# Kernel tuning notes

Hardware: AMD Instinct MI355X
Metric: run time of the kernel (lower is better)

Reference implementation:

```python
import jax, jax.numpy as jnp
import numpy as np

N, IN_DIM, INTER, HID, OUT, G = 8192, 512, 512, 1024, 512, 16
EPS = 1e-5


def setup_inputs() -> dict:
    key = jax.random.key(0)
    ks = jax.random.split(key, 16)
    s = 0.02
    return {
        "h": jax.random.normal(ks[0], (N, IN_DIM), jnp.float32),
        "D": jax.random.uniform(ks[1], (N, N), jnp.float32),
        "h_prime": jax.random.normal(ks[2], (N, OUT), jnp.float32),
        "Qw": jax.random.normal(ks[3], (IN_DIM, INTER), jnp.float32) * s,
        "Qb": jnp.zeros((INTER,), jnp.float32),
        "Kw": jax.random.normal(ks[4], (IN_DIM, INTER), jnp.float32) * s,
        "Kb": jnp.zeros((INTER,), jnp.float32),
        "Vw": jax.random.normal(ks[5], (IN_DIM, INTER), jnp.float32) * s,
        "Vb": jnp.zeros((INTER,), jnp.float32),
        "Rw": jax.random.normal(ks[6], (INTER, HID), jnp.float32) * s,
        "Rb": jnp.zeros((HID,), jnp.float32),
        "Cw": jax.random.normal(ks[7], (OUT, HID), jnp.float32) * s,
        "Cb": jnp.zeros((HID,), jnp.float32),
        "Pw": jax.random.normal(ks[8], (2 * HID, OUT), jnp.float32) * s,
        "Pb": jnp.zeros((OUT,), jnp.float32),
        "prelu_a": jnp.full((OUT,), 0.25, jnp.float32),  # PReLU default init
        "gn_w": jnp.ones((OUT,), jnp.float32),
        "gn_b": jnp.zeros((OUT,), jnp.float32),
    }


def reference(h, D, h_prime, Qw, Qb, Kw, Kb, Vw, Vb, Rw, Rb, Cw, Cb, Pw, Pb, prelu_a, gn_w, gn_b):
    Q = h @ Qw + Qb                      # (N, inter)
    K = h @ Kw + Kb
    V = h @ Vw + Vb
    scores = D * (Q @ K.T)               # (N, N), decayed retention scores
    h_ret = scores @ V                   # (N, inter)
    h_ret = jax.nn.gelu(h_ret @ Rw + Rb, approximate=False)   # (N, hid)
    h_cat = h_prime @ Cw + Cb            # (N, hid)
    combined = jnp.concatenate([h_ret, h_cat], axis=-1)       # (N, 2*hid)
    x = combined @ Pw + Pb               # (N, out)
    x = jnp.where(x >= 0, x, prelu_a * x)                      # PReLU per-channel
    # GroupNorm over channel groups per row: (N, G, out/G)
    xg = x.reshape(N, G, OUT // G)
    mu = xg.mean(axis=-1, keepdims=True)
    var = xg.var(axis=-1, keepdims=True)
    xn = ((xg - mu) * jax.lax.rsqrt(var + EPS)).reshape(N, OUT)
    return xn * gn_w + gn_b
```

## Files before the change

### kernel.cpp

```cpp
#include <hip/hip_runtime.h>
#include <math.h>

typedef __attribute__((ext_vector_type(8))) short bf16x8;
typedef __attribute__((ext_vector_type(4))) float f32x4;
typedef __attribute__((ext_vector_type(8))) unsigned short u16x8;

#define DEVFN __device__ __forceinline__

DEVFN unsigned short f2bf(float f) {
    unsigned int u = __float_as_uint(f);
    u += 0x7fffu + ((u >> 16) & 1u);
    return (unsigned short)(u >> 16);
}

__global__ void cast_f32_bf16_kernel(const float* __restrict__ in,
                                     unsigned short* __restrict__ out, int n8) {
    int i = blockIdx.x * blockDim.x + threadIdx.x;
    if (i >= n8) return;
    const float4* p = reinterpret_cast<const float4*>(in) + (size_t)i * 2;
    float4 a = p[0], b = p[1];
    u16x8 o;
    o[0] = f2bf(a.x); o[1] = f2bf(a.y); o[2] = f2bf(a.z); o[3] = f2bf(a.w);
    o[4] = f2bf(b.x); o[5] = f2bf(b.y); o[6] = f2bf(b.z); o[7] = f2bf(b.w);
    reinterpret_cast<u16x8*>(out)[i] = o;
}

__global__ void sum4_cast_kernel(const float* __restrict__ p, size_t stride,
                                 unsigned short* __restrict__ out, int n8) {
    int i = blockIdx.x * blockDim.x + threadIdx.x;
    if (i >= n8) return;
    const float4* a = reinterpret_cast<const float4*>(p) + (size_t)i * 2;
    const float4* b = reinterpret_cast<const float4*>(p + stride) + (size_t)i * 2;
    const float4* c = reinterpret_cast<const float4*>(p + 2 * stride) + (size_t)i * 2;
    const float4* d = reinterpret_cast<const float4*>(p + 3 * stride) + (size_t)i * 2;
    u16x8 o;
#pragma unroll
    for (int j = 0; j < 2; ++j) {
        float4 va = a[j], vb = b[j], vc = c[j], vd = d[j];
        o[4 * j + 0] = f2bf(va.x + vb.x + vc.x + vd.x);
        o[4 * j + 1] = f2bf(va.y + vb.y + vc.y + vd.y);
        o[4 * j + 2] = f2bf(va.z + vb.z + vc.z + vd.z);
        o[4 * j + 3] = f2bf(va.w + vb.w + vc.w + vd.w);
    }
    reinterpret_cast<u16x8*>(out)[i] = o;
}

__global__ void concat_bias_kernel(const float* __restrict__ a,
                                   const float* __restrict__ b,
                                   const float* __restrict__ c,
                                   float* __restrict__ o) {
    int i = blockIdx.x * blockDim.x + threadIdx.x;
    if (i >= 1536) return;
    o[i] = i < 512 ? a[i] : (i < 1024 ? b[i - 512] : c[i - 1024]);
}

DEVFN unsigned short to_bf16_bits(float f) { return f2bf(f); }
DEVFN unsigned short to_bf16_bits(unsigned short u) { return u; }

template <typename T>
__global__ void transpose_to_bf16_kernel(const T* __restrict__ in, int ldin,
                                         unsigned short* __restrict__ out, int ldout) {
    __shared__ unsigned short tile[32][34];
    int c0 = blockIdx.x * 32, r0 = blockIdx.y * 32;
    int tx = threadIdx.x, ty = threadIdx.y;
#pragma unroll
    for (int i = 0; i < 32; i += 8)
        tile[ty + i][tx] = to_bf16_bits(in[(size_t)(r0 + ty + i) * ldin + c0 + tx]);
    __syncthreads();
#pragma unroll
    for (int i = 0; i < 32; i += 8)
        out[(size_t)(c0 + ty + i) * ldout + r0 + tx] = tile[tx][ty + i];
}

enum { EP_BF16_BIAS = 0, EP_BF16_DMUL = 1, EP_BF16_GELU = 2, EP_F32 = 3, EP_PRELU_GN = 4 };

template <int MODE>
__global__ __launch_bounds__(256) void gemm_bt_kernel(
    const unsigned short* __restrict__ A, int lda,
    const unsigned short* __restrict__ B, int ldb,
    void* __restrict__ Cv, int ldc, int K,
    const float* __restrict__ bias,
    const float* __restrict__ Dmul, int ldd,
    const float* __restrict__ PA, const float* __restrict__ GW,
    const float* __restrict__ GB, size_t zstride) {
    __shared__ alignas(16) unsigned short As[128 * 64];
    __shared__ alignas(16) unsigned short Bs[128 * 64];

    unsigned nwg = gridDim.x * gridDim.y;
    unsigned bid = blockIdx.y * gridDim.x + blockIdx.x;
    unsigned cpx = nwg >> 3;
    bid = (bid & 7u) * cpx + (bid >> 3);
    unsigned bx = bid % gridDim.x, by = bid / gridDim.x;
    size_t m0 = (size_t)by * 128, n0 = (size_t)bx * 128;

    size_t koff = (size_t)blockIdx.z * K;
    A += koff;
    B += koff;

    int tid = threadIdx.x;
    int lane = tid & 63, w = tid >> 6;
    int wr = w >> 1, wc = w & 1;

    f32x4 acc[4][4];
#pragma unroll
    for (int i = 0; i < 4; ++i)
#pragma unroll
        for (int j = 0; j < 4; ++j)
#pragma unroll
            for (int r = 0; r < 4; ++r) acc[i][j][r] = 0.f;

    const unsigned short* Ablk = A + m0 * lda;
    const unsigned short* Bblk = B + n0 * ldb;
    int srccol = ((lane & 7) ^ (lane >> 3)) * 8;
    int srow = w * 32 + (lane >> 3);
    unsigned short* ldsA = As + w * 2048;
    unsigned short* ldsB = Bs + w * 2048;

    int nkt = K >> 6;
    for (int kt = 0; kt < nkt; ++kt) {
        int k0 = kt << 6;
#pragma unroll
        for (int i = 0; i < 4; ++i) {
            __builtin_amdgcn_global_load_lds(
                (const __attribute__((address_space(1))) void*)(Ablk + (size_t)(srow + i * 8) * lda + k0 + srccol),
                (__attribute__((address_space(3))) void*)(ldsA + i * 512), 16, 0, 0);
            __builtin_amdgcn_global_load_lds(
                (const __attribute__((address_space(1))) void*)(Bblk + (size_t)(srow + i * 8) * ldb + k0 + srccol),
                (__attribute__((address_space(3))) void*)(ldsB + i * 512), 16, 0, 0);
        }
        __syncthreads();

        const bf16x8* Ap = reinterpret_cast<const bf16x8*>(As);
        const bf16x8* Bp = reinterpret_cast<const bf16x8*>(Bs);
#pragma unroll
        for (int kk = 0; kk < 2; ++kk) {
            bf16x8 af[4], bfr[4];
#pragma unroll
            for (int mi = 0; mi < 4; ++mi) {
                int row = wr * 64 + mi * 16 + (lane & 15);
                int slot = ((kk << 2) + (lane >> 4)) ^ (row & 7);
                af[mi] = Ap[row * 8 + slot];
            }
#pragma unroll
            for (int ni = 0; ni < 4; ++ni) {
                int row = wc * 64 + ni * 16 + (lane & 15);
                int slot = ((kk << 2) + (lane >> 4)) ^ (row & 7);
                bfr[ni] = Bp[row * 8 + slot];
            }
#pragma unroll
            for (int mi = 0; mi < 4; ++mi)
#pragma unroll
                for (int ni = 0; ni < 4; ++ni)
                    acc[mi][ni] = __builtin_amdgcn_mfma_f32_16x16x32_bf16(
                        af[mi], bfr[ni], acc[mi][ni], 0, 0, 0);
        }
        __syncthreads();
    }

    int cif = lane & 15;
    int rif = (lane >> 4) << 2;

    if (MODE == EP_PRELU_GN) {
        float* Cf = (float*)Cv;
        float pbv[4], pav[4], gwv[4], gbv[4];
        size_t gcolv[4];
#pragma unroll
        for (int ni = 0; ni < 4; ++ni) {
            gcolv[ni] = n0 + wc * 64 + ni * 16 + cif;
            pbv[ni] = bias[gcolv[ni]];
            pav[ni] = PA[gcolv[ni]];
            gwv[ni] = GW[gcolv[ni]];
            gbv[ni] = GB[gcolv[ni]];
        }
#pragma unroll
        for (int mi = 0; mi < 4; ++mi) {
#pragma unroll
            for (int ni = 0; ni < 4; ++ni)
#pragma unroll
                for (int r = 0; r < 4; ++r) {
                    float v = acc[mi][ni][r] + pbv[ni];
                    acc[mi][ni][r] = v >= 0.f ? v : pav[ni] * v;
                }
#pragma unroll
            for (int p = 0; p < 2; ++p) {
                float s[4], ss[4];
#pragma unroll
                for (int r = 0; r < 4; ++r) {
                    float a0 = acc[mi][2 * p][r], a1 = acc[mi][2 * p + 1][r];
                    s[r] = a0 + a1;
                    ss[r] = a0 * a0 + a1 * a1;
                }
#pragma unroll
                for (int msk = 1; msk < 16; msk <<= 1)
#pragma unroll
                    for (int r = 0; r < 4; ++r) {
                        s[r] += __shfl_xor(s[r], msk);
                        ss[r] += __shfl_xor(ss[r], msk);
                    }
#pragma unroll
                for (int r = 0; r < 4; ++r) {
                    float mu = s[r] * (1.f / 32.f);
                    float inv = rsqrtf(ss[r] * (1.f / 32.f) - mu * mu + 1e-5f);
                    size_t grow = m0 + wr * 64 + mi * 16 + rif + r;
#pragma unroll
                    for (int q = 0; q < 2; ++q) {
                        int ni = 2 * p + q;
                        Cf[grow * (size_t)ldc + gcolv[ni]] =
                            (acc[mi][ni][r] - mu) * inv * gwv[ni] + gbv[ni];
                    }
                }
            }
        }
        return;
    }

#pragma unroll
    for (int mi = 0; mi < 4; ++mi) {
#pragma unroll
        for (int ni = 0; ni < 4; ++ni) {
            size_t gcol = n0 + wc * 64 + ni * 16 + cif;
            float bval = 0.f;
            if (MODE == EP_BF16_BIAS || MODE == EP_BF16_GELU || MODE == EP_F32)
                if (bias) bval = bias[gcol];
#pragma unroll
            for (int r = 0; r < 4; ++r) {
                size_t grow = m0 + wr * 64 + mi * 16 + rif + r;
                float val = acc[mi][ni][r] + bval;
                if (MODE == EP_BF16_DMUL)
                    val = acc[mi][ni][r] * Dmul[grow * (size_t)ldd + gcol];
                if (MODE == EP_BF16_GELU)
                    val = 0.5f * val * (1.f + erff(val * 0.70710678118654752f));
                if (MODE == EP_F32) {
                    float* Cf = (float*)Cv + blockIdx.z * zstride;
                    Cf[grow * (size_t)ldc + gcol] = val;
                } else {
                    ((unsigned short*)Cv)[grow * (size_t)ldc + gcol] = f2bf(val);
                }
            }
        }
    }
}

extern "C" void kernel_launch(void* const* d_in, const int* in_sizes, int n_in,
                              void* d_out, int out_size, void* d_ws, size_t ws_size,
                              hipStream_t stream) {
    constexpr int Nn = 8192, IND = 512, INTER = 512, HID = 1024, OUTD = 512;
    const float* h   = (const float*)d_in[0];
    const float* Dm  = (const float*)d_in[1];
    const float* hp  = (const float*)d_in[2];
    const float* Qw  = (const float*)d_in[3];
    const float* Qb  = (const float*)d_in[4];
    const float* Kw  = (const float*)d_in[5];
    const float* Kb  = (const float*)d_in[6];
    const float* Vw  = (const float*)d_in[7];
    const float* Vb  = (const float*)d_in[8];
    const float* Rw  = (const float*)d_in[9];
    const float* Rb  = (const float*)d_in[10];
    const float* Cw  = (const float*)d_in[11];
    const float* Cb  = (const float*)d_in[12];
    const float* Pw  = (const float*)d_in[13];
    const float* Pb  = (const float*)d_in[14];
    const float* pa  = (const float*)d_in[15];
    const float* gwt = (const float*)d_in[16];
    const float* gbt = (const float*)d_in[17];
    (void)in_sizes; (void)n_in; (void)out_size; (void)ws_size;

    char* ws = (char*)d_ws;
    size_t cur = 0;
    auto alloc = [&](size_t bytes) -> void* {
        void* p = ws + cur;
        cur += (bytes + 255) & ~(size_t)255;
        return p;
    };
    unsigned short* h_bf   = (unsigned short*)alloc((size_t)Nn * IND * 2);
    unsigned short* hp_bf  = (unsigned short*)alloc((size_t)Nn * OUTD * 2);
    unsigned short* QKVwT  = (unsigned short*)alloc((size_t)3 * INTER * IND * 2);
    float*          qkvb   = (float*)alloc((size_t)3 * INTER * 4);
    unsigned short* RwT    = (unsigned short*)alloc((size_t)INTER * HID * 2);
    unsigned short* CwT    = (unsigned short*)alloc((size_t)OUTD * HID * 2);
    unsigned short* PwT    = (unsigned short*)alloc((size_t)2 * HID * OUTD * 2);
    unsigned short* QKVm   = (unsigned short*)alloc((size_t)Nn * 3 * INTER * 2);
    unsigned short* VTm    = (unsigned short*)alloc((size_t)Nn * INTER * 2);
    unsigned short* Sm     = (unsigned short*)alloc((size_t)Nn * Nn * 2);
    float*          hret32 = (float*)alloc((size_t)4 * Nn * INTER * 4);
    unsigned short* hretbf = (unsigned short*)alloc((size_t)Nn * INTER * 2);
    unsigned short* comb   = Sm;

    unsigned short* Qm = QKVm;
    unsigned short* Km = QKVm + INTER;
    unsigned short* Vm = QKVm + 2 * INTER;
    const int ldqkv = 3 * INTER;

    dim3 tb(32, 8);
    int n8 = Nn * IND / 8;
    cast_f32_bf16_kernel<<<n8 / 256, 256, 0, stream>>>(h, h_bf, n8);
    cast_f32_bf16_kernel<<<n8 / 256, 256, 0, stream>>>(hp, hp_bf, n8);
    transpose_to_bf16_kernel<float><<<dim3(INTER / 32, IND / 32), tb, 0, stream>>>(Qw, INTER, QKVwT, IND);
    transpose_to_bf16_kernel<float><<<dim3(INTER / 32, IND / 32), tb, 0, stream>>>(Kw, INTER, QKVwT + (size_t)INTER * IND, IND);
    transpose_to_bf16_kernel<float><<<dim3(INTER / 32, IND / 32), tb, 0, stream>>>(Vw, INTER, QKVwT + (size_t)2 * INTER * IND, IND);
    concat_bias_kernel<<<6, 256, 0, stream>>>(Qb, Kb, Vb, qkvb);
    transpose_to_bf16_kernel<float><<<dim3(HID / 32, INTER / 32), tb, 0, stream>>>(Rw, HID, RwT, INTER);
    transpose_to_bf16_kernel<float><<<dim3(HID / 32, OUTD / 32), tb, 0, stream>>>(Cw, HID, CwT, OUTD);
    transpose_to_bf16_kernel<float><<<dim3(OUTD / 32, 2 * HID / 32), tb, 0, stream>>>(Pw, OUTD, PwT, 2 * HID);

    gemm_bt_kernel<EP_BF16_BIAS><<<dim3(3 * INTER / 128, Nn / 128), 256, 0, stream>>>(
        h_bf, IND, QKVwT, IND, QKVm, ldqkv, IND, qkvb, nullptr, 0, nullptr, nullptr, nullptr, 0);
    transpose_to_bf16_kernel<unsigned short><<<dim3(INTER / 32, Nn / 32), tb, 0, stream>>>(Vm, ldqkv, VTm, Nn);

    gemm_bt_kernel<EP_BF16_DMUL><<<dim3(Nn / 128, Nn / 128), 256, 0, stream>>>(
        Qm, ldqkv, Km, ldqkv, Sm, Nn, INTER, nullptr, Dm, Nn, nullptr, nullptr, nullptr, 0);

    gemm_bt_kernel<EP_F32><<<dim3(OUTD / 128, Nn / 128, 4), 256, 0, stream>>>(
        Sm, Nn, VTm, Nn, hret32, INTER, Nn / 4, nullptr, nullptr, 0,
        nullptr, nullptr, nullptr, (size_t)Nn * INTER);
    sum4_cast_kernel<<<(Nn * INTER / 8) / 256, 256, 0, stream>>>(
        hret32, (size_t)Nn * INTER, hretbf, Nn * INTER / 8);

    gemm_bt_kernel<EP_BF16_GELU><<<dim3(HID / 128, Nn / 128), 256, 0, stream>>>(
        hretbf, INTER, RwT, INTER, comb, 2 * HID, INTER, Rb, nullptr, 0, nullptr, nullptr, nullptr, 0);
    gemm_bt_kernel<EP_BF16_BIAS><<<dim3(HID / 128, Nn / 128), 256, 0, stream>>>(
        hp_bf, OUTD, CwT, OUTD, comb + HID, 2 * HID, OUTD, Cb, nullptr, 0, nullptr, nullptr, nullptr, 0);

    gemm_bt_kernel<EP_PRELU_GN><<<dim3(OUTD / 128, Nn / 128), 256, 0, stream>>>(
        comb, 2 * HID, PwT, 2 * HID, d_out, OUTD, 2 * HID, Pb, nullptr, 0, pa, gwt, gbt, 0);
}
```

Baseline: 450.7 us.

## Double-buffer GEMM LDS, prefetch D, merge launches, remap split-K blocks

The GEMM kernel now double-buffers its LDS tiles so the next K-tile's global-to-LDS loads overlap the MFMA work on the current tile. In the score GEMM, the D-matrix elements are prefetched into registers during the last K iteration instead of being loaded in the epilogue. Split-K blocks are remapped across XCDs, and launch_bounds now requests 2 blocks per CU. Several small launches are merged: two casts into one, six weight transposes into one, and the R and C GEMMs into a single dual-mode launch. This doubles LDS use to 64KB per block and adds 64 prefetch registers per thread, which may limit occupancy.

```diff
diff --git a/kernel.cpp b/kernel.cpp
--- a/kernel.cpp
+++ b/kernel.cpp
@@ -13,15 +13,18 @@
     return (unsigned short)(u >> 16);
 }
 
-__global__ void cast_f32_bf16_kernel(const float* __restrict__ in,
-                                     unsigned short* __restrict__ out, int n8) {
+__global__ void cast2_kernel(const float* __restrict__ a, const float* __restrict__ b,
+                             unsigned short* __restrict__ oa, unsigned short* __restrict__ ob,
+                             int n8) {
+    const float* in = blockIdx.y ? b : a;
+    unsigned short* out = blockIdx.y ? ob : oa;
     int i = blockIdx.x * blockDim.x + threadIdx.x;
     if (i >= n8) return;
     const float4* p = reinterpret_cast<const float4*>(in) + (size_t)i * 2;
-    float4 a = p[0], b = p[1];
+    float4 x = p[0], y = p[1];
     u16x8 o;
-    o[0] = f2bf(a.x); o[1] = f2bf(a.y); o[2] = f2bf(a.z); o[3] = f2bf(a.w);
-    o[4] = f2bf(b.x); o[5] = f2bf(b.y); o[6] = f2bf(b.z); o[7] = f2bf(b.w);
+    o[0] = f2bf(x.x); o[1] = f2bf(x.y); o[2] = f2bf(x.z); o[3] = f2bf(x.w);
+    o[4] = f2bf(y.x); o[5] = f2bf(y.y); o[6] = f2bf(y.z); o[7] = f2bf(y.w);
     reinterpret_cast<u16x8*>(out)[i] = o;
 }
 
@@ -54,52 +57,97 @@
     o[i] = i < 512 ? a[i] : (i < 1024 ? b[i - 512] : c[i - 1024]);
 }
 
-DEVFN unsigned short to_bf16_bits(float f) { return f2bf(f); }
-DEVFN unsigned short to_bf16_bits(unsigned short u) { return u; }
-
-template <typename T>
-__global__ void transpose_to_bf16_kernel(const T* __restrict__ in, int ldin,
-                                         unsigned short* __restrict__ out, int ldout) {
+struct TD { const float* in; unsigned short* out; int ldin, ldout, nbx, nby; };
+struct TD6 { TD d[6]; };
+
+__global__ void multi_transpose_kernel(TD6 t6) {
+    TD d = t6.d[blockIdx.z];
+    if ((int)blockIdx.x >= d.nbx || (int)blockIdx.y >= d.nby) return;
     __shared__ unsigned short tile[32][34];
     int c0 = blockIdx.x * 32, r0 = blockIdx.y * 32;
     int tx = threadIdx.x, ty = threadIdx.y;
 #pragma unroll
     for (int i = 0; i < 32; i += 8)
-        tile[ty + i][tx] = to_bf16_bits(in[(size_t)(r0 + ty + i) * ldin + c0 + tx]);
+        tile[ty + i][tx] = f2bf(d.in[(size_t)(r0 + ty + i) * d.ldin + c0 + tx]);
+    __syncthreads();
+#pragma unroll
+    for (int i = 0; i < 32; i += 8)
+        d.out[(size_t)(c0 + ty + i) * d.ldout + r0 + tx] = tile[tx][ty + i];
+}
+
+__global__ void transpose_bf16_kernel(const unsigned short* __restrict__ in, int ldin,
+                                      unsigned short* __restrict__ out, int ldout) {
+    __shared__ unsigned short tile[32][34];
+    int c0 = blockIdx.x * 32, r0 = blockIdx.y * 32;
+    int tx = threadIdx.x, ty = threadIdx.y;
+#pragma unroll
+    for (int i = 0; i < 32; i += 8)
+        tile[ty + i][tx] = in[(size_t)(r0 + ty + i) * ldin + c0 + tx];
     __syncthreads();
 #pragma unroll
     for (int i = 0; i < 32; i += 8)
         out[(size_t)(c0 + ty + i) * ldout + r0 + tx] = tile[tx][ty + i];
 }
 
-enum { EP_BF16_BIAS = 0, EP_BF16_DMUL = 1, EP_BF16_GELU = 2, EP_F32 = 3, EP_PRELU_GN = 4 };
+enum { EP_BF16_BIAS = 0, EP_BF16_DMUL = 1, EP_F32 = 3, EP_PRELU_GN = 4, EP_DUAL = 5 };
 
 template <int MODE>
-__global__ __launch_bounds__(256) void gemm_bt_kernel(
+__global__ __launch_bounds__(256, 2) void gemm_bt_kernel(
     const unsigned short* __restrict__ A, int lda,
     const unsigned short* __restrict__ B, int ldb,
     void* __restrict__ Cv, int ldc, int K,
     const float* __restrict__ bias,
     const float* __restrict__ Dmul, int ldd,
     const float* __restrict__ PA, const float* __restrict__ GW,
-    const float* __restrict__ GB, size_t zstride) {
-    __shared__ alignas(16) unsigned short As[128 * 64];
-    __shared__ alignas(16) unsigned short Bs[128 * 64];
-
-    unsigned nwg = gridDim.x * gridDim.y;
-    unsigned bid = blockIdx.y * gridDim.x + blockIdx.x;
-    unsigned cpx = nwg >> 3;
-    bid = (bid & 7u) * cpx + (bid >> 3);
-    unsigned bx = bid % gridDim.x, by = bid / gridDim.x;
-    size_t m0 = (size_t)by * 128, n0 = (size_t)bx * 128;
-
-    size_t koff = (size_t)blockIdx.z * K;
-    A += koff;
-    B += koff;
+    const float* __restrict__ GB, size_t zstride,
+    const unsigned short* __restrict__ A2,
+    const unsigned short* __restrict__ B2,
+    const float* __restrict__ bias2) {
+    __shared__ alignas(16) unsigned short As[2][128 * 64];
+    __shared__ alignas(16) unsigned short Bs[2][128 * 64];
+
+    unsigned bx, by, zi;
+    if (MODE == EP_F32) {
+        unsigned gx = gridDim.x;
+        unsigned L = (blockIdx.z * gridDim.y + blockIdx.y) * gx + blockIdx.x;
+        unsigned xcd = L & 7u, slot = L >> 3;
+        zi = xcd >> 1;
+        unsigned t = slot * 2 + (xcd & 1u);
+        bx = t & (gx - 1);
+        by = t / gx;
+    } else {
+        unsigned nwg = gridDim.x * gridDim.y;
+        unsigned bid = blockIdx.y * gridDim.x + blockIdx.x;
+        unsigned cpx = nwg >> 3;
+        bid = (bid & 7u) * cpx + (bid >> 3);
+        bx = bid % gridDim.x;
+        by = bid / gridDim.x;
+        zi = 0;
+    }
+    size_t m0 = (size_t)by * 128;
+    size_t nB = (size_t)bx * 128;
+    size_t ncol0 = nB;
+
+    const unsigned short* Ause = A;
+    const unsigned short* Buse = B;
+    const float* bias_use = bias;
+    bool apply_gelu = false;
+    if (MODE == EP_DUAL) {
+        unsigned half = gridDim.x >> 1;
+        if (bx >= half) {
+            nB = (size_t)(bx - half) * 128;
+            ncol0 = 1024 + nB;
+            Ause = A2; Buse = B2; bias_use = bias2;
+        } else {
+            apply_gelu = true;
+        }
+    }
 
     int tid = threadIdx.x;
     int lane = tid & 63, w = tid >> 6;
     int wr = w >> 1, wc = w & 1;
+    int cif = lane & 15;
+    int rif = (lane >> 4) << 2;
 
     f32x4 acc[4][4];
 #pragma unroll
@@ -109,29 +157,50 @@
 #pragma unroll
             for (int r = 0; r < 4; ++r) acc[i][j][r] = 0.f;
 
-    const unsigned short* Ablk = A + m0 * lda;
-    const unsigned short* Bblk = B + n0 * ldb;
+    const unsigned short* Ablk = Ause + m0 * lda + (size_t)zi * K;
+    const unsigned short* Bblk = Buse + nB * ldb + (size_t)zi * K;
     int srccol = ((lane & 7) ^ (lane >> 3)) * 8;
     int srow = w * 32 + (lane >> 3);
-    unsigned short* ldsA = As + w * 2048;
-    unsigned short* ldsB = Bs + w * 2048;
-
     int nkt = K >> 6;
-    for (int kt = 0; kt < nkt; ++kt) {
+
+    float dreg[4][4][4];
+
+    auto stage = [&](int buf, int kt) {
         int k0 = kt << 6;
+        unsigned short* la = &As[buf][w * 2048];
+        unsigned short* lb = &Bs[buf][w * 2048];
 #pragma unroll
         for (int i = 0; i < 4; ++i) {
             __builtin_amdgcn_global_load_lds(
                 (const __attribute__((address_space(1))) void*)(Ablk + (size_t)(srow + i * 8) * lda + k0 + srccol),
-                (__attribute__((address_space(3))) void*)(ldsA + i * 512), 16, 0, 0);
+                (__attribute__((address_space(3))) void*)(la + i * 512), 16, 0, 0);
             __builtin_amdgcn_global_load_lds(
                 (const __attribute__((address_space(1))) void*)(Bblk + (size_t)(srow + i * 8) * ldb + k0 + srccol),
-                (__attribute__((address_space(3))) void*)(ldsB + i * 512), 16, 0, 0);
-        }
-        __syncthreads();
-
-        const bf16x8* Ap = reinterpret_cast<const bf16x8*>(As);
-        const bf16x8* Bp = reinterpret_cast<const bf16x8*>(Bs);
+                (__attribute__((address_space(3))) void*)(lb + i * 512), 16, 0, 0);
+        }
+    };
+
+    stage(0, 0);
+    __syncthreads();
+
+    for (int kt = 0; kt < nkt; ++kt) {
+        int cur = kt & 1;
+        if (kt + 1 < nkt) {
+            stage(cur ^ 1, kt + 1);
+        } else if (MODE == EP_BF16_DMUL) {
+#pragma unroll
+            for (int mi = 0; mi < 4; ++mi)
+#pragma unroll
+                for (int ni = 0; ni < 4; ++ni)
+#pragma unroll
+                    for (int r = 0; r < 4; ++r)
+                        dreg[mi][ni][r] =
+                            Dmul[(m0 + wr * 64 + mi * 16 + rif + r) * (size_t)ldd +
+                                 (ncol0 + wc * 64 + ni * 16 + cif)];
+        }
+
+        const bf16x8* Ap = reinterpret_cast<const bf16x8*>(As[cur]);
+        const bf16x8* Bp = reinterpret_cast<const bf16x8*>(Bs[cur]);
 #pragma unroll
         for (int kk = 0; kk < 2; ++kk) {
             bf16x8 af[4], bfr[4];
@@ -157,16 +226,13 @@
         __syncthreads();
     }
 
-    int cif = lane & 15;
-    int rif = (lane >> 4) << 2;
-
     if (MODE == EP_PRELU_GN) {
         float* Cf = (float*)Cv;
         float pbv[4], pav[4], gwv[4], gbv[4];
         size_t gcolv[4];
 #pragma unroll
         for (int ni = 0; ni < 4; ++ni) {
-            gcolv[ni] = n0 + wc * 64 + ni * 16 + cif;
+            gcolv[ni] = ncol0 + wc * 64 + ni * 16 + cif;
             pbv[ni] = bias[gcolv[ni]];
             pav[ni] = PA[gcolv[ni]];
             gwv[ni] = GW[gcolv[ni]];
@@ -218,20 +284,21 @@
     for (int mi = 0; mi < 4; ++mi) {
 #pragma unroll
         for (int ni = 0; ni < 4; ++ni) {
-            size_t gcol = n0 + wc * 64 + ni * 16 + cif;
+            size_t gcol = ncol0 + wc * 64 + ni * 16 + cif;
+            size_t bcol = nB + wc * 64 + ni * 16 + cif;
             float bval = 0.f;
-            if (MODE == EP_BF16_BIAS || MODE == EP_BF16_GELU || MODE == EP_F32)
-                if (bias) bval = bias[gcol];
+            if (MODE == EP_BF16_BIAS || MODE == EP_DUAL || MODE == EP_F32)
+                if (bias_use) bval = bias_use[bcol];
 #pragma unroll
             for (int r = 0; r < 4; ++r) {
                 size_t grow = m0 + wr * 64 + mi * 16 + rif + r;
                 float val = acc[mi][ni][r] + bval;
                 if (MODE == EP_BF16_DMUL)
-                    val = acc[mi][ni][r] * Dmul[grow * (size_t)ldd + gcol];
-                if (MODE == EP_BF16_GELU)
+                    val = acc[mi][ni][r] * dreg[mi][ni][r];
+                if (MODE == EP_DUAL && apply_gelu)
                     val = 0.5f * val * (1.f + erff(val * 0.70710678118654752f));
                 if (MODE == EP_F32) {
-                    float* Cf = (float*)Cv + blockIdx.z * zstride;
+                    float* Cf = (float*)Cv + zi * zstride;
                     Cf[grow * (size_t)ldc + gcol] = val;
                 } else {
                     ((unsigned short*)Cv)[grow * (size_t)ldc + gcol] = f2bf(val);
@@ -293,34 +360,38 @@
 
     dim3 tb(32, 8);
     int n8 = Nn * IND / 8;
-    cast_f32_bf16_kernel<<<n8 / 256, 256, 0, stream>>>(h, h_bf, n8);
-    cast_f32_bf16_kernel<<<n8 / 256, 256, 0, stream>>>(hp, hp_bf, n8);
-    transpose_to_bf16_kernel<float><<<dim3(INTER / 32, IND / 32), tb, 0, stream>>>(Qw, INTER, QKVwT, IND);
-    transpose_to_bf16_kernel<float><<<dim3(INTER / 32, IND / 32), tb, 0, stream>>>(Kw, INTER, QKVwT + (size_t)INTER * IND, IND);
-    transpose_to_bf16_kernel<float><<<dim3(INTER / 32, IND / 32), tb, 0, stream>>>(Vw, INTER, QKVwT + (size_t)2 * INTER * IND, IND);
+    cast2_kernel<<<dim3(n8 / 256, 2), 256, 0, stream>>>(h, hp, h_bf, hp_bf, n8);
+
+    TD6 t6;
+    t6.d[0] = {Qw, QKVwT,                          INTER, IND,     16, 16};
+    t6.d[1] = {Kw, QKVwT + (size_t)INTER * IND,    INTER, IND,     16, 16};
+    t6.d[2] = {Vw, QKVwT + (size_t)2 * INTER * IND,INTER, IND,     16, 16};
+    t6.d[3] = {Rw, RwT,                            HID,   INTER,   32, 16};
+    t6.d[4] = {Cw, CwT,                            HID,   OUTD,    32, 16};
+    t6.d[5] = {Pw, PwT,                            OUTD,  2 * HID, 16, 64};
+    multi_transpose_kernel<<<dim3(32, 64, 6), tb, 0, stream>>>(t6);
     concat_bias_kernel<<<6, 256, 0, stream>>>(Qb, Kb, Vb, qkvb);
-    transpose_to_bf16_kernel<float><<<dim3(HID / 32, INTER / 32), tb, 0, stream>>>(Rw, HID, RwT, INTER);
-    transpose_to_bf16_kernel<float><<<dim3(HID / 32, OUTD / 32), tb, 0, stream>>>(Cw, HID, CwT, OUTD);
-    transpose_to_bf16_kernel<float><<<dim3(OUTD / 32, 2 * HID / 32), tb, 0, stream>>>(Pw, OUTD, PwT, 2 * HID);
 
     gemm_bt_kernel<EP_BF16_BIAS><<<dim3(3 * INTER / 128, Nn / 128), 256, 0, stream>>>(
-        h_bf, IND, QKVwT, IND, QKVm, ldqkv, IND, qkvb, nullptr, 0, nullptr, nullptr, nullptr, 0);
-    transpose_to_bf16_kernel<unsigned short><<<dim3(INTER / 32, Nn / 32), tb, 0, stream>>>(Vm, ldqkv, VTm, Nn);
+        h_bf, IND, QKVwT, IND, QKVm, ldqkv, IND, qkvb, nullptr, 0,
+        nullptr, nullptr, nullptr, 0, nullptr, nullptr, nullptr);
+    transpose_bf16_kernel<<<dim3(INTER / 32, Nn / 32), tb, 0, stream>>>(Vm, ldqkv, VTm, Nn);
 
     gemm_bt_kernel<EP_BF16_DMUL><<<dim3(Nn / 128, Nn / 128), 256, 0, stream>>>(
-        Qm, ldqkv, Km, ldqkv, Sm, Nn, INTER, nullptr, Dm, Nn, nullptr, nullptr, nullptr, 0);
+        Qm, ldqkv, Km, ldqkv, Sm, Nn, INTER, nullptr, Dm, Nn,
+        nullptr, nullptr, nullptr, 0, nullptr, nullptr, nullptr);
 
     gemm_bt_kernel<EP_F32><<<dim3(OUTD / 128, Nn / 128, 4), 256, 0, stream>>>(
         Sm, Nn, VTm, Nn, hret32, INTER, Nn / 4, nullptr, nullptr, 0,
-        nullptr, nullptr, nullptr, (size_t)Nn * INTER);
+        nullptr, nullptr, nullptr, (size_t)Nn * INTER, nullptr, nullptr, nullptr);
     sum4_cast_kernel<<<(Nn * INTER / 8) / 256, 256, 0, stream>>>(
         hret32, (size_t)Nn * INTER, hretbf, Nn * INTER / 8);
 
-    gemm_bt_kernel<EP_BF16_GELU><<<dim3(HID / 128, Nn / 128), 256, 0, stream>>>(
-        hretbf, INTER, RwT, INTER, comb, 2 * HID, INTER, Rb, nullptr, 0, nullptr, nullptr, nullptr, 0);
-    gemm_bt_kernel<EP_BF16_BIAS><<<dim3(HID / 128, Nn / 128), 256, 0, stream>>>(
-        hp_bf, OUTD, CwT, OUTD, comb + HID, 2 * HID, OUTD, Cb, nullptr, 0, nullptr, nullptr, nullptr, 0);
+    gemm_bt_kernel<EP_DUAL><<<dim3(2 * HID / 128, Nn / 128), 256, 0, stream>>>(
+        hretbf, INTER, RwT, INTER, comb, 2 * HID, INTER, Rb, nullptr, 0,
+        nullptr, nullptr, nullptr, 0, hp_bf, CwT, Cb);
 
     gemm_bt_kernel<EP_PRELU_GN><<<dim3(OUTD / 128, Nn / 128), 256, 0, stream>>>(
-        comb, 2 * HID, PwT, 2 * HID, d_out, OUTD, 2 * HID, Pb, nullptr, 0, pa, gwt, gbt, 0);
-}
+        comb, 2 * HID, PwT, 2 * HID, d_out, OUTD, 2 * HID, Pb, nullptr, 0,
+        pa, gwt, gbt, 0, nullptr, nullptr, nullptr);
+}
```

Result: faster. 422.6 us (-6.2%).
